# Optimization experiments

Measured on AMD Instinct MI355X. Metric: run time of the kernel, lower is better.

The kernel has to match this reference:

```python
import jax, jax.numpy as jnp
import numpy as np

# static config (mirrors init_kwargs)
B, IMG_C, IN_C, OUT_C, S = 16, 3, 256, 512, 128
HIDDEN = IN_C                     # min(out_dim, in_dim) in DepthwiseSynthesisKernel
KGEN_IN = 32                      # (3+1)//2 * 4 * (512//128)
KSIZE = 3                         # generated depthwise kernel taps (= conv_kernel)
NUM_TAPS = KGEN_IN - 2 * KSIZE + 2  # 28, low-pass filter taps
CUTOFF, HALFWIDTH = 32.0, 7.35
CONV_CLAMP = 256.0
LRELU_GAIN = float(np.sqrt(2.0))  # bias_act def_gain for lrelu
DN = ('NCHW', 'OIHW', 'NCHW')

def _firwin(numtaps, cutoff, width, fs):
    # numpy re-implementation of scipy.signal.firwin (kaiser window, lowpass)
    nyq = fs / 2.0
    atten = 2.285 * (numtaps - 1) * np.pi * (width / nyq) + 7.95
    if atten > 50:
        beta = 0.1102 * (atten - 8.7)
    elif atten > 21:
        beta = 0.5842 * (atten - 21) ** 0.4 + 0.07886 * (atten - 21)
    else:
        beta = 0.0
    m = np.arange(numtaps) - (numtaps - 1) / 2.0
    c = cutoff / nyq
    h = c * np.sinc(c * m) * np.kaiser(numtaps, beta)
    return (h / h.sum()).astype(np.float32)

def setup_inputs():
    key = jax.random.key(0)
    ks = jax.random.split(key, 9)
    img = jax.random.normal(ks[0], (B, IMG_C, S, S), jnp.float32)
    fromrgb_w = jax.random.normal(ks[1], (IN_C, IMG_C, 1, 1), jnp.float32)
    fromrgb_b = jnp.zeros((IN_C,), jnp.float32)
    freqs = jax.random.normal(ks[2], (HIDDEN, 2), jnp.float32)
    radii = jnp.sqrt(jnp.sum(freqs ** 2, axis=1, keepdims=True))
    freqs = freqs / (radii * jnp.exp(radii ** 2) ** 0.25) * 8.0  # w0_init = 8
    phases = jax.random.uniform(ks[3], (HIDDEN,), jnp.float32) - 0.5
    hz_outdim = jax.random.normal(ks[4], (IN_C, HIDDEN), jnp.float32)
    vt_outdim = jax.random.normal(ks[5], (IN_C, HIDDEN), jnp.float32)
    gauss_sigma = jnp.ones((), jnp.float32)
    lr_weight0 = jax.random.normal(ks[6], (IN_C, IN_C, 1, 1), jnp.float32) / np.sqrt(IN_C)
    point_w = jax.random.normal(ks[7], (OUT_C, IN_C, 1, 1), jnp.float32)
    point_b = jnp.zeros((OUT_C,), jnp.float32)
    low_filter = jnp.asarray(_firwin(NUM_TAPS, CUTOFF, HALFWIDTH * 2, CUTOFF * 2 ** 1.1))
    gauss_x = jnp.arange(KGEN_IN, dtype=jnp.float32) - (KGEN_IN - 1) / 2.0
    fir = jnp.array([1.0, 3.0, 3.0, 1.0], jnp.float32)
    fir = fir / fir.sum()  # upfirdn2d.setup_filter normalization
    return dict(img=img, fromrgb_w=fromrgb_w, fromrgb_b=fromrgb_b, freqs=freqs,
                phases=phases, hz_outdim=hz_outdim, vt_outdim=vt_outdim,
                gauss_sigma=gauss_sigma, lr_weight0=lr_weight0, point_w=point_w,
                point_b=point_b, low_filter=low_filter, gauss_x=gauss_x, fir=fir)

def _conv(x, w, stride=(1, 1), pad=((0, 0), (0, 0)), groups=1):
    return jax.lax.conv_general_dilated(x, w, stride, pad,
                                        feature_group_count=groups,
                                        dimension_numbers=DN)

def _bias_act(x, b, act, gain, clamp):
    x = x + b[None, :, None, None]
    if act == 'lrelu':
        x = jnp.where(x >= 0, x, 0.2 * x)
    x = x * gain
    return jnp.clip(x, -clamp, clamp)

def _sample_weight(grid, coeff, gauss_sigma, gauss_x, low_filter):
    # grid: [HIDDEN, KGEN_IN], coeff: [IN_C, HIDDEN] -> [IN_C, KSIZE]
    basis = jnp.sin(grid * (2.0 * jnp.pi)) * np.float32(np.exp(-0.5))  # density = 1
    w = jnp.einsum('cg,ic->ig', basis, coeff) / np.float32(np.sqrt(HIDDEN))
    w = w - w.mean()
    w = w * jax.lax.rsqrt(jnp.mean(w * w, axis=0, keepdims=True) + 1e-8)
    gs = 1.0 + gauss_sigma ** 2 / 5.0
    w = w * jnp.exp(-(gauss_x ** 2) / (2.0 * gs))
    # valid 1D correlation with low-pass filter, then stride-2 pick
    w = jax.lax.conv_general_dilated(w[:, None, :], low_filter[None, None, :], (1,),
                                     [(0, 0)], dimension_numbers=('NCH', 'OIH', 'NCH'))[:, 0, :]
    return w[:, ::2]

def _forward(img, fromrgb_w, fromrgb_b, freqs, phases, hz_outdim, vt_outdim,
             gauss_sigma, lr_weight0, point_w, point_b, low_filter, gauss_x, fir):
    # fromrgb: Conv2dLayer(act='linear') applies sin() to input, then conv + bias + clamp
    x = jnp.sin(img)
    x = _conv(x, fromrgb_w * np.float32(1.0 / np.sqrt(IMG_C)))  # weight_gain 1/sqrt(in*k^2)
    x = _bias_act(x, fromrgb_b, 'linear', 1.0, CONV_CLAMP)
    # conv0_gen: generate separable depthwise kernels
    g = (jnp.arange(KGEN_IN, dtype=jnp.float32) - (KGEN_IN - 1) / 2.0) * (2.0 / (KGEN_IN + 1))
    hz = _sample_weight(freqs[:, 0:1] * g[None, :] + phases[:, None], hz_outdim,
                        gauss_sigma, gauss_x, low_filter)  # [IN_C, 3]
    vt = _sample_weight(freqs[:, 1:2] * g[None, :] + phases[:, None], vt_outdim,
                        gauss_sigma, gauss_x, low_filter)
    gdw = np.float32(1.0 / np.sqrt(KSIZE))  # Conv2dWrapper weight_gain, I=1, kHkW=3
    y = _conv(x, (vt * gdw).reshape(IN_C, 1, KSIZE, 1), pad=((1, 1), (0, 0)), groups=IN_C)
    y = _conv(y, (hz * gdw).reshape(IN_C, 1, 1, KSIZE), pad=((0, 0), (1, 1)), groups=IN_C)
    # low-rank 1x1 residual path (lr_weight0 via Conv2dWrapper: extra 1/sqrt(IN_C) gain)
    y = y + _conv(x, lr_weight0 * np.float32(1.0 / np.sqrt(IN_C)))
    # conv0_point: 1x1, lrelu, gain sqrt(2), clamp
    y = _conv(y, point_w * np.float32(1.0 / np.sqrt(IN_C)))
    y = _bias_act(y, point_b, 'lrelu', LRELU_GAIN, CONV_CLAMP)
    # FIR downsample by 2 with separable [1,3,3,1]/8 filter (upfirdn2d.downsample2d)
    fv = jnp.broadcast_to(fir.reshape(1, 1, 4, 1), (OUT_C, 1, 4, 1))
    fh = jnp.broadcast_to(fir.reshape(1, 1, 1, 4), (OUT_C, 1, 1, 4))
    y = _conv(y, fv, stride=(2, 1), pad=((1, 1), (0, 0)), groups=OUT_C)
    y = _conv(y, fh, stride=(1, 2), pad=((0, 0), (1, 1)), groups=OUT_C)
    return y  # [B, OUT_C, S//2, S//2]

def reference(img, fromrgb_w, fromrgb_b, freqs, phases, hz_outdim, vt_outdim,
              gauss_sigma, lr_weight0, point_w, point_b, low_filter, gauss_x, fir):
    return _forward(img, fromrgb_w, fromrgb_b, freqs, phases, hz_outdim, vt_outdim,
                    gauss_sigma, lr_weight0, point_w, point_b, low_filter, gauss_x, fir)
```

## Files before the change

### kernel.cpp

```cpp
#include <hip/hip_runtime.h>

typedef __attribute__((ext_vector_type(4))) float f32x4;
typedef __attribute__((ext_vector_type(8))) short s16x8;
typedef unsigned short u16;

#define KGEN 32
#define NTAPS 28

__device__ __forceinline__ float bf2f(u16 v) {
    return __uint_as_float(((unsigned)v) << 16);
}
__device__ __forceinline__ u16 f2bf(float f) {
    unsigned u = __float_as_uint(f);
    unsigned r = (u + 0x7fffu + ((u >> 16) & 1u)) >> 16;
    return (u16)r;
}

#define ASYNC_COPY16(gptr, lptr)                                               \
    __builtin_amdgcn_global_load_lds(                                          \
        (const __attribute__((address_space(1))) unsigned int*)(gptr),         \
        (__attribute__((address_space(3))) unsigned int*)(lptr), 16, 0, 0)

__global__ __launch_bounds__(256) void prep_kernel(
    const float* __restrict__ freqs, const float* __restrict__ phases,
    const float* __restrict__ hz_outdim, const float* __restrict__ vt_outdim,
    const float* __restrict__ gsig, const float* __restrict__ low_filter,
    const float* __restrict__ gauss_x, float* __restrict__ hzvt,
    const float* __restrict__ point_w, const float* __restrict__ lr_w,
    u16* __restrict__ wcat,
    const float* __restrict__ img, const float* __restrict__ frw,
    const float* __restrict__ frb, u16* __restrict__ xu)
{
    __shared__ union {
        struct {
            float basis[256][KGEN];
            float red[256];
            float colscale[KGEN];
        } g;
        float pw[256];
        struct {
            float sins[3][32];
            float wT[3][264];
            float bT[264];
        } f;
    } sm;

    const int bidx = blockIdx.x;
    const int t = threadIdx.x;

    if (bidx < 2) {
        const int which = bidx;
        const int i = t;
        {
            float f = freqs[i * 2 + which];
            float p = phases[i];
            #pragma unroll
            for (int j = 0; j < KGEN; j++) {
                float g = ((float)j - 15.5f) * (2.0f / 33.0f);
                sm.g.basis[i][j] = __sinf((f * g + p) * 6.283185307179586f) * 0.6065306597126334f;
            }
        }
        __syncthreads();

        const float* coeff = (which == 0) ? hz_outdim : vt_outdim;
        float acc[KGEN];
        #pragma unroll
        for (int j = 0; j < KGEN; j++) acc[j] = 0.f;

        const float4* crow = (const float4*)(coeff + (size_t)i * 256);
        for (int c4 = 0; c4 < 64; c4++) {
            float4 cv = crow[c4];
            int c = c4 * 4;
            #pragma unroll
            for (int j = 0; j < KGEN; j++) {
                acc[j] += sm.g.basis[c][j] * cv.x + sm.g.basis[c + 1][j] * cv.y
                        + sm.g.basis[c + 2][j] * cv.z + sm.g.basis[c + 3][j] * cv.w;
            }
        }
        #pragma unroll
        for (int j = 0; j < KGEN; j++) acc[j] *= 0.0625f;

        float s = 0.f;
        #pragma unroll
        for (int j = 0; j < KGEN; j++) s += acc[j];
        sm.g.red[i] = s;
        __syncthreads();
        for (int st = 128; st > 0; st >>= 1) {
            if (i < st) sm.g.red[i] += sm.g.red[i + st];
            __syncthreads();
        }
        float mean = sm.g.red[0] * (1.0f / 8192.0f);
        #pragma unroll
        for (int j = 0; j < KGEN; j++) acc[j] -= mean;

        #pragma unroll
        for (int j = 0; j < KGEN; j++) sm.g.basis[i][j] = acc[j];
        __syncthreads();
        if (i < KGEN) {
            float ss = 0.f;
            for (int r = 0; r < 256; r++) { float v = sm.g.basis[r][i]; ss += v * v; }
            sm.g.colscale[i] = rsqrtf(ss * (1.0f / 256.0f) + 1e-8f);
        }
        __syncthreads();

        float sg = gsig[0];
        float gs = 1.0f + sg * sg * 0.2f;
        #pragma unroll
        for (int j = 0; j < KGEN; j++) {
            float gx = gauss_x[j];
            acc[j] = acc[j] * sm.g.colscale[j] * expf(-(gx * gx) / (2.0f * gs));
        }

        float lf[NTAPS];
        #pragma unroll
        for (int tt = 0; tt < NTAPS; tt++) lf[tt] = low_filter[tt];
        #pragma unroll
        for (int p = 0; p < 3; p++) {
            int t0 = 2 * p;
            float o = 0.f;
            #pragma unroll
            for (int tt = 0; tt < NTAPS; tt++) o += acc[t0 + tt] * lf[tt];
            hzvt[((size_t)which * 256 + i) * 3 + p] = o;
        }
    } else if (bidx < 514) {
        const int n = bidx - 2;
        const int j = t;
        sm.pw[j] = point_w[(size_t)n * 256 + j];
        __syncthreads();
        float a0 = 0.f, a1 = 0.f, a2 = 0.f, a3 = 0.f;
        for (int c = 0; c < 256; c += 4) {
            a0 += sm.pw[c + 0] * lr_w[(size_t)(c + 0) * 256 + j];
            a1 += sm.pw[c + 1] * lr_w[(size_t)(c + 1) * 256 + j];
            a2 += sm.pw[c + 2] * lr_w[(size_t)(c + 2) * 256 + j];
            a3 += sm.pw[c + 3] * lr_w[(size_t)(c + 3) * 256 + j];
        }
        float acc = (a0 + a1) + (a2 + a3);
        wcat[(size_t)n * 512 + j]       = f2bf(sm.pw[j] * 0.0625f);
        wcat[(size_t)n * 512 + 256 + j] = f2bf(acc * (1.0f / 256.0f));
    } else {
        const int pos_base = (bidx - 514) * 32;
        const int b = pos_base >> 14;
        const int hw = pos_base & 16383;

        if (t < 96) {
            const int ch = t >> 5, p = t & 31;
            sm.f.sins[ch][p] = __sinf(img[((size_t)b * 3 + ch) * 16384 + hw + p]);
        }
        for (int idx = t; idx < 768; idx += 256) {
            const int c = idx / 3, k = idx - c * 3;
            sm.f.wT[k][c + (c >> 5)] = frw[idx];
        }
        sm.f.bT[t + (t >> 5)] = frb[t];
        __syncthreads();

        const int p = t >> 3;
        const int g8 = t & 7;
        const int c0 = g8 * 32;
        const float s0 = sm.f.sins[0][p];
        const float s1 = sm.f.sins[1][p];
        const float s2 = sm.f.sins[2][p];
        const float gn = 0.5773502691896258f;

        u16* dst = xu + (size_t)(pos_base + p) * 512 + 256 + c0;
        #pragma unroll
        for (int q0 = 0; q0 < 4; q0++) {
            union { u16 q[8]; s16x8 v; } ov;
            #pragma unroll
            for (int q = 0; q < 8; q++) {
                const int cp = c0 + q0 * 8 + q + g8;
                float v = (s0 * sm.f.wT[0][cp] + s1 * sm.f.wT[1][cp]
                         + s2 * sm.f.wT[2][cp]) * gn + sm.f.bT[cp];
                v = fminf(256.f, fmaxf(-256.f, v));
                ov.q[q] = f2bf(v);
            }
            *(s16x8*)(dst + q0 * 8) = ov.v;
        }
    }
}

__global__ __launch_bounds__(256) void dw_kernel(
    u16* __restrict__ xu, const float* __restrict__ hzvt)
{
    const int t = threadIdx.x;
    const int c0 = (t & 31) * 8;
    const int wq = t >> 5;
    const int pos0 = blockIdx.x * 32 + wq * 4;
    const int w0 = pos0 & 127;
    const int h = (pos0 >> 7) & 127;
    const int b = pos0 >> 14;

    union { float4 v[6]; float f[24]; } hzw, vtw;
    const float4* hp = (const float4*)(hzvt + (size_t)c0 * 3);
    const float4* vp = (const float4*)(hzvt + 768 + (size_t)c0 * 3);
    #pragma unroll
    for (int q = 0; q < 6; q++) { hzw.v[q] = hp[q]; vtw.v[q] = vp[q]; }

    float acc[4][8];
    #pragma unroll
    for (int o = 0; o < 4; o++)
        #pragma unroll
        for (int q = 0; q < 8; q++) acc[o][q] = 0.f;

    #pragma unroll
    for (int i = 0; i < 3; i++) {
        int hh = h + i - 1;
        if (hh < 0 || hh > 127) continue;
        float w2[3][8];
        #pragma unroll
        for (int q = 0; q < 8; q++) {
            const float vq = vtw.f[q * 3 + i];
            w2[0][q] = vq * hzw.f[q * 3 + 0];
            w2[1][q] = vq * hzw.f[q * 3 + 1];
            w2[2][q] = vq * hzw.f[q * 3 + 2];
        }
        const u16* rowp = xu + ((size_t)((b * 128 + hh) * 128) * 512) + 256 + c0;
        #pragma unroll
        for (int dx = 0; dx < 6; dx++) {
            const int ww = w0 + dx - 1;
            s16x8 xv;
            if (ww >= 0 && ww <= 127) xv = *(const s16x8*)(rowp + (size_t)ww * 512);
            else xv = (s16x8){0,0,0,0,0,0,0,0};
            float xf[8];
            #pragma unroll
            for (int q = 0; q < 8; q++) xf[q] = bf2f((u16)xv[q]);
            #pragma unroll
            for (int o = 0; o < 4; o++) {
                const int j = dx - o;
                if (j < 0 || j > 2) continue;
                #pragma unroll
                for (int q = 0; q < 8; q++) acc[o][q] += w2[j][q] * xf[q];
            }
        }
    }

    #pragma unroll
    for (int o = 0; o < 4; o++) {
        union { u16 q[8]; s16x8 v; } ov;
        #pragma unroll
        for (int q = 0; q < 8; q++) ov.q[q] = f2bf(acc[o][q] * (1.0f / 3.0f));
        *(s16x8*)(xu + (size_t)(pos0 + o) * 512 + c0) = ov.v;
    }
}

__global__ __launch_bounds__(256) void gemm_kernel(
    const u16* __restrict__ xu, const u16* __restrict__ wcat,
    const float* __restrict__ point_b, u16* __restrict__ ypre, int nofs)
{
    __shared__ u16 smem[16384];
    u16* As = smem;
    u16* Bs = smem + 8192;

    const int tid = threadIdx.x;
    const int bid = blockIdx.x;
    const int ntile = (bid >> 3) & 1;
    const int mtile = (bid & 7) | ((bid >> 4) << 3);

    const int srow = tid >> 3;
    const int slot = tid & 7;
    const int ek = slot ^ (srow & 7);
    const size_t abase = (size_t)(mtile * 128 + srow) * 512 + ek * 8;
    const int nbase = nofs + ntile * 128;
    const size_t bbase = (size_t)(nbase + srow) * 512 + ek * 8;
    u16* asdst = &As[(size_t)tid * 8];
    u16* bsdst = &Bs[(size_t)tid * 8];

    const int lane = tid & 63;
    const int wave = tid >> 6;
    const int wm = (wave >> 1) * 64;
    const int wn = (wave & 1) * 64;
    const int l16 = lane & 15;
    const int lq = lane >> 4;

    f32x4 acc[4][4];
    #pragma unroll
    for (int a = 0; a < 4; a++)
        #pragma unroll
        for (int c = 0; c < 4; c++) acc[a][c] = (f32x4){0.f, 0.f, 0.f, 0.f};

    for (int kt = 0; kt < 8; kt++) {
        __syncthreads();
        const int ko = kt * 64;
        #pragma unroll
        for (int i = 0; i < 4; i++) {
            ASYNC_COPY16(xu + abase + (size_t)i * 32 * 512 + ko, asdst + i * 2048);
            ASYNC_COPY16(wcat + bbase + (size_t)i * 32 * 512 + ko, bsdst + i * 2048);
        }
        __syncthreads();

        #pragma unroll
        for (int kk = 0; kk < 2; kk++) {
            s16x8 af[4], bf[4];
            #pragma unroll
            for (int mi = 0; mi < 4; mi++) {
                const int r = wm + mi * 16 + l16;
                af[mi] = *(const s16x8*)&As[r * 64 + (((kk * 4 + lq) ^ (r & 7)) * 8)];
            }
            #pragma unroll
            for (int ni = 0; ni < 4; ni++) {
                const int r = wn + ni * 16 + l16;
                bf[ni] = *(const s16x8*)&Bs[r * 64 + (((kk * 4 + lq) ^ (r & 7)) * 8)];
            }
            #pragma unroll
            for (int mi = 0; mi < 4; mi++)
                #pragma unroll
                for (int ni = 0; ni < 4; ni++)
                    acc[mi][ni] = __builtin_amdgcn_mfma_f32_16x16x32_bf16(
                        af[mi], bf[ni], acc[mi][ni], 0, 0, 0);
        }
    }

    __syncthreads();
    #pragma unroll
    for (int ni = 0; ni < 4; ni++) {
        const int nloc = wn + ni * 16 + l16;
        const float bias = point_b[nofs + ntile * 128 + nloc];
        #pragma unroll
        for (int mi = 0; mi < 4; mi++) {
            const int m0 = wm + mi * 16 + lq * 4;
            union { u16 q[4]; uint2 d; } pk;
            #pragma unroll
            for (int r = 0; r < 4; r++) {
                float v = acc[mi][ni][r] + bias;
                v = (v >= 0.f) ? v : 0.2f * v;
                v *= 1.4142135623730951f;
                v = fminf(256.f, fmaxf(-256.f, v));
                pk.q[r] = f2bf(v);
            }
            const int chunk = m0 >> 3;
            const int within = m0 & 7;
            const int sl = chunk ^ (nloc & 7);
            *(uint2*)&smem[nloc * 128 + sl * 8 + within] = pk.d;
        }
    }
    __syncthreads();

    const int b = mtile >> 7;
    const int h = mtile & 127;
    const int nl2 = tid >> 1;
    const int halfsel = tid & 1;
    const int nl = ntile * 128 + nl2;
    u16* drow = ypre + ((size_t)(b * 256 + nl) * 128 + h) * 128;
    #pragma unroll
    for (int j = 0; j < 8; j++) {
        const int c = halfsel * 8 + j;
        const int sl = c ^ (nl2 & 7);
        uint4 v = *(const uint4*)&smem[nl2 * 128 + sl * 8];
        *(uint4*)(drow + c * 8) = v;
    }
}

__global__ __launch_bounds__(256) void fir_kernel(
    const u16* __restrict__ ypre, const float* __restrict__ fir,
    float* __restrict__ out, int nofs)
{
    const int bid = blockIdx.x;
    const int tid = threadIdx.x;
    const int lane = tid & 63;
    const int wave = tid >> 6;
    const int ohhalf = bid & 1;
    const int nl = (bid >> 1) & 255;
    const int b = bid >> 9;
    const u16* src = ypre + (size_t)(b * 256 + nl) * 16384;
    float* dst = out + (size_t)(b * 512 + nofs + nl) * 4096;

    const float f0 = fir[0], f1 = fir[1], f2 = fir[2], f3 = fir[3];

    auto hrow = [&](int r) -> float {
        if (r < 0 || r > 127) return 0.f;
        unsigned raw = *(const unsigned*)(src + (size_t)r * 128 + lane * 2);
        float y0 = bf2f((u16)(raw & 0xffffu));
        float y1 = bf2f((u16)(raw >> 16));
        float ym = __shfl_up(y1, 1u);
        if (lane == 0) ym = 0.f;
        float yp = __shfl_down(y0, 1u);
        if (lane == 63) yp = 0.f;
        return f0 * ym + f1 * y0 + f2 * y1 + f3 * yp;
    };

    const int oh0 = ohhalf * 32 + wave * 8;
    float A = hrow(2 * oh0 - 1);
    float Bv = hrow(2 * oh0);
    for (int oh = oh0; oh < oh0 + 8; oh++) {
        float C = hrow(2 * oh + 1);
        float D = hrow(2 * oh + 2);
        dst[oh * 64 + lane] = f0 * A + f1 * Bv + f2 * C + f3 * D;
        A = C;
        Bv = D;
    }
}

extern "C" void kernel_launch(void* const* d_in, const int* in_sizes, int n_in,
                              void* d_out, int out_size, void* d_ws, size_t ws_size,
                              hipStream_t stream)
{
    (void)in_sizes; (void)n_in; (void)out_size; (void)ws_size;
    const float* img        = (const float*)d_in[0];
    const float* fromrgb_w  = (const float*)d_in[1];
    const float* fromrgb_b  = (const float*)d_in[2];
    const float* freqs      = (const float*)d_in[3];
    const float* phases     = (const float*)d_in[4];
    const float* hz_outdim  = (const float*)d_in[5];
    const float* vt_outdim  = (const float*)d_in[6];
    const float* gsig       = (const float*)d_in[7];
    const float* lr_w       = (const float*)d_in[8];
    const float* point_w    = (const float*)d_in[9];
    const float* point_b    = (const float*)d_in[10];
    const float* low_filter = (const float*)d_in[11];
    const float* gauss_x    = (const float*)d_in[12];
    const float* fir        = (const float*)d_in[13];

    char* ws = (char*)d_ws;
    u16*   xu   = (u16*)(ws);
    u16*   ypre = (u16*)(ws + 268435456LL);
    u16*   wcat = (u16*)(ws + 402653184LL);
    float* hzvt = (float*)(ws + 403177472LL);
    float* out  = (float*)d_out;

    hipLaunchKernelGGL(prep_kernel, dim3(8706), dim3(256), 0, stream,
                       freqs, phases, hz_outdim, vt_outdim, gsig, low_filter, gauss_x, hzvt,
                       point_w, lr_w, wcat, img, fromrgb_w, fromrgb_b, xu);
    hipLaunchKernelGGL(dw_kernel, dim3(8192), dim3(256), 0, stream,
                       xu, hzvt);
    for (int half = 0; half < 2; half++) {
        hipLaunchKernelGGL(gemm_kernel, dim3(4096), dim3(256), 0, stream,
                           xu, wcat, point_b, ypre, half * 256);
        hipLaunchKernelGGL(fir_kernel, dim3(8192), dim3(256), 0, stream,
                           ypre, fir, out, half * 256);
    }
}
```

Baseline: 677.8 us.

## Keep full-K weight tile resident in LDS and stream A directly from global

The GEMM kernel now loads a 64-row, full-K (512) slice of the weight matrix into LDS once per block, then each wave reads its A fragments straight from global memory with no per-K-step staging or barriers. The tile shape changes from 128x128 to 256x64 per block, with each wave owning 64 rows. The epilogue uses a per-wave padded LDS staging buffer for the transposed stores. This removes the eight K-loop barrier pairs and the A staging, at the cost of uncoalesced global A loads, more blocks re-reading A across N tiles, and 64KB of LDS per block, which limits occupancy.

```diff
diff --git a/kernel.cpp b/kernel.cpp
--- a/kernel.cpp
+++ b/kernel.cpp
@@ -246,77 +246,74 @@
     const u16* __restrict__ xu, const u16* __restrict__ wcat,
     const float* __restrict__ point_b, u16* __restrict__ ypre, int nofs)
 {
-    __shared__ u16 smem[16384];
-    u16* As = smem;
-    u16* Bs = smem + 8192;
+    __shared__ u16 Bs[64 * 512];
 
     const int tid = threadIdx.x;
     const int bid = blockIdx.x;
-    const int ntile = (bid >> 3) & 1;
-    const int mtile = (bid & 7) | ((bid >> 4) << 3);
-
-    const int srow = tid >> 3;
-    const int slot = tid & 7;
-    const int ek = slot ^ (srow & 7);
-    const size_t abase = (size_t)(mtile * 128 + srow) * 512 + ek * 8;
-    const int nbase = nofs + ntile * 128;
-    const size_t bbase = (size_t)(nbase + srow) * 512 + ek * 8;
-    u16* asdst = &As[(size_t)tid * 8];
-    u16* bsdst = &Bs[(size_t)tid * 8];
-
     const int lane = tid & 63;
     const int wave = tid >> 6;
-    const int wm = (wave >> 1) * 64;
-    const int wn = (wave & 1) * 64;
     const int l16 = lane & 15;
     const int lq = lane >> 4;
 
+    const int tt = bid >> 3;
+    const int ntile = tt & 3;
+    const int mt = ((tt >> 2) << 3) | (bid & 7);
+
+    const int n0 = nofs + ntile * 64;
+
+    {
+        const int r0 = wave * 16;
+        #pragma unroll
+        for (int rr = 0; rr < 16; rr++) {
+            const int n = r0 + rr;
+            const u16* gp = wcat + (size_t)(n0 + n) * 512 + ((lane ^ (n & 7)) * 8);
+            ASYNC_COPY16(gp, &Bs[n * 512 + lane * 8]);
+        }
+    }
+    __syncthreads();
+
+    const int mbase = mt * 256 + wave * 64;
+    const u16* ap[4];
+    #pragma unroll
+    for (int mi = 0; mi < 4; mi++)
+        ap[mi] = xu + (size_t)(mbase + mi * 16 + l16) * 512 + lq * 8;
+
     f32x4 acc[4][4];
     #pragma unroll
     for (int a = 0; a < 4; a++)
         #pragma unroll
         for (int c = 0; c < 4; c++) acc[a][c] = (f32x4){0.f, 0.f, 0.f, 0.f};
 
-    for (int kt = 0; kt < 8; kt++) {
-        __syncthreads();
-        const int ko = kt * 64;
-        #pragma unroll
-        for (int i = 0; i < 4; i++) {
-            ASYNC_COPY16(xu + abase + (size_t)i * 32 * 512 + ko, asdst + i * 2048);
-            ASYNC_COPY16(wcat + bbase + (size_t)i * 32 * 512 + ko, bsdst + i * 2048);
-        }
-        __syncthreads();
-
-        #pragma unroll
-        for (int kk = 0; kk < 2; kk++) {
-            s16x8 af[4], bf[4];
-            #pragma unroll
-            for (int mi = 0; mi < 4; mi++) {
-                const int r = wm + mi * 16 + l16;
-                af[mi] = *(const s16x8*)&As[r * 64 + (((kk * 4 + lq) ^ (r & 7)) * 8)];
-            }
-            #pragma unroll
-            for (int ni = 0; ni < 4; ni++) {
-                const int r = wn + ni * 16 + l16;
-                bf[ni] = *(const s16x8*)&Bs[r * 64 + (((kk * 4 + lq) ^ (r & 7)) * 8)];
-            }
-            #pragma unroll
-            for (int mi = 0; mi < 4; mi++)
-                #pragma unroll
-                for (int ni = 0; ni < 4; ni++)
-                    acc[mi][ni] = __builtin_amdgcn_mfma_f32_16x16x32_bf16(
-                        af[mi], bf[ni], acc[mi][ni], 0, 0, 0);
-        }
+    #pragma unroll
+    for (int kq = 0; kq < 16; kq++) {
+        s16x8 af[4], bf[4];
+        #pragma unroll
+        for (int mi = 0; mi < 4; mi++)
+            af[mi] = *(const s16x8*)(ap[mi] + kq * 32);
+        #pragma unroll
+        for (int ni = 0; ni < 4; ni++) {
+            const int n = ni * 16 + l16;
+            const int c = kq * 4 + lq;
+            bf[ni] = *(const s16x8*)&Bs[n * 512 + ((c ^ (n & 7)) * 8)];
+        }
+        #pragma unroll
+        for (int mi = 0; mi < 4; mi++)
+            #pragma unroll
+            for (int ni = 0; ni < 4; ni++)
+                acc[mi][ni] = __builtin_amdgcn_mfma_f32_16x16x32_bf16(
+                    af[mi], bf[ni], acc[mi][ni], 0, 0, 0);
     }
 
     __syncthreads();
+    u16* ep = &Bs[wave * (64 * 68)];
+
     #pragma unroll
     for (int ni = 0; ni < 4; ni++) {
-        const int nloc = wn + ni * 16 + l16;
-        const float bias = point_b[nofs + ntile * 128 + nloc];
+        const int n = ni * 16 + l16;
+        const float bias = point_b[n0 + n];
         #pragma unroll
         for (int mi = 0; mi < 4; mi++) {
-            const int m0 = wm + mi * 16 + lq * 4;
+            const int m0 = mi * 16 + lq * 4;
             union { u16 q[4]; uint2 d; } pk;
             #pragma unroll
             for (int r = 0; r < 4; r++) {
@@ -326,26 +323,23 @@
                 v = fminf(256.f, fmaxf(-256.f, v));
                 pk.q[r] = f2bf(v);
             }
-            const int chunk = m0 >> 3;
-            const int within = m0 & 7;
-            const int sl = chunk ^ (nloc & 7);
-            *(uint2*)&smem[nloc * 128 + sl * 8 + within] = pk.d;
+            *(uint2*)&ep[n * 68 + m0] = pk.d;
         }
     }
     __syncthreads();
 
-    const int b = mtile >> 7;
-    const int h = mtile & 127;
-    const int nl2 = tid >> 1;
-    const int halfsel = tid & 1;
-    const int nl = ntile * 128 + nl2;
-    u16* drow = ypre + ((size_t)(b * 256 + nl) * 128 + h) * 128;
-    #pragma unroll
-    for (int j = 0; j < 8; j++) {
-        const int c = halfsel * 8 + j;
-        const int sl = c ^ (nl2 & 7);
-        uint4 v = *(const uint4*)&smem[nl2 * 128 + sl * 8];
-        *(uint4*)(drow + c * 8) = v;
+    const int b = mt >> 6;
+    const int h = ((mt & 63) << 1) | (wave >> 1);
+    const int w0 = (wave & 1) * 64;
+    const int nr = lane >> 3;
+    const int j = lane & 7;
+    #pragma unroll
+    for (int g = 0; g < 8; g++) {
+        const int n = g * 8 + nr;
+        uint4 v = *(const uint4*)&ep[n * 68 + j * 8];
+        const int nloc = ntile * 64 + n;
+        u16* dst = ypre + ((size_t)(b * 256 + nloc) * 128 + h) * 128 + w0 + j * 8;
+        *(uint4*)dst = v;
     }
 }
 
```

After: 771.2 us. 13.8% more time.
